# Optimization experiments

Hardware: AMD Instinct MI355X
Metric: run time of the kernel (lower is better)

## Reference

```python
import jax, jax.numpy as jnp
import numpy as np

S, N, H = 1024, 64, 1024  # source len, batch, hidden_size
INPUT_SIZE = 1024         # attention projection dim (linear1/linear2 out)


def setup_inputs() -> dict:
    key = jax.random.key(0)
    ks = jax.random.split(key, 8)
    sc_h = 1.0 / np.sqrt(H)
    sc_i = 1.0 / np.sqrt(INPUT_SIZE)
    return {
        "out_e": jax.random.normal(ks[0], (S, N, H), dtype=jnp.float32),
        "hidden_d": jax.random.normal(ks[1], (1, N, H), dtype=jnp.float32),
        # torch Linear weights are [out_features, in_features]
        "W1": jax.random.uniform(ks[2], (INPUT_SIZE, H), jnp.float32, -sc_h, sc_h),
        "b1": jax.random.uniform(ks[3], (INPUT_SIZE,), jnp.float32, -sc_h, sc_h),
        "W2": jax.random.uniform(ks[4], (INPUT_SIZE, H), jnp.float32, -sc_h, sc_h),
        "b2": jax.random.uniform(ks[5], (INPUT_SIZE,), jnp.float32, -sc_h, sc_h),
        "W3": jax.random.uniform(ks[6], (1, INPUT_SIZE), jnp.float32, -sc_i, sc_i),
        "b3": jax.random.uniform(ks[7], (1,), jnp.float32, -sc_i, sc_i),
    }


def reference(out_e, hidden_d, W1, b1, W2, b2, W3, b3):
    # hidden_d [1,N,H] broadcast to [S,N,H] (torch .repeat)
    s = out_e.shape[0]
    hd = jnp.broadcast_to(hidden_d, (s,) + hidden_d.shape[1:])
    # a: [S,N,1] = linear3(tanh(linear1(hd) + linear2(out_e)))
    e = jnp.tanh(hd @ W1.T + b1 + out_e @ W2.T + b2)
    a = e @ W3.T + b3
    # softmax over the source dim (dim=0 in torch)
    alpha = jax.nn.softmax(a, axis=0)          # [S,N,1]
    c = jnp.einsum('sne,snh->enh', alpha, out_e)  # [1,N,H]
    return (c, alpha)
```

## Files before the change

kernel.cpp:

```cpp
#include <hip/hip_runtime.h>
#include <hip/hip_fp16.h>

#define S_LEN 1024
#define N_B   64
#define H_DIM 1024
#define I_DIM 1024

typedef __attribute__((ext_vector_type(8))) _Float16 half8;
typedef __attribute__((ext_vector_type(4))) _Float16 half4;
typedef __attribute__((ext_vector_type(4))) float    f32x4;

__device__ __forceinline__ void gload16(const void* g, void* l) {
  __builtin_amdgcn_global_load_lds(
      (const __attribute__((address_space(1))) unsigned int*)g,
      (__attribute__((address_space(3))) unsigned int*)l, 16, 0, 0);
}

__global__ void cvt_f32_f16(const float* __restrict__ src,
                            _Float16* __restrict__ dst, int n8) {
  int idx = blockIdx.x * blockDim.x + threadIdx.x;
  int stride = gridDim.x * blockDim.x;
  const float4* s4 = (const float4*)src;
  half8* d8 = (half8*)dst;
  for (int i = idx; i < n8; i += stride) {
    float4 a = s4[2 * i], b = s4[2 * i + 1];
    half8 h;
    h[0] = (_Float16)a.x; h[1] = (_Float16)a.y;
    h[2] = (_Float16)a.z; h[3] = (_Float16)a.w;
    h[4] = (_Float16)b.x; h[5] = (_Float16)b.y;
    h[6] = (_Float16)b.z; h[7] = (_Float16)b.w;
    d8[i] = h;
  }
}

__global__ void u1_kernel(const float* __restrict__ hd,
                          const float* __restrict__ W1,
                          const float* __restrict__ b1,
                          const float* __restrict__ b2,
                          float* __restrict__ u1,
                          float* __restrict__ a_ws) {
  __shared__ float hs[4 * 1024];
  int nb = blockIdx.x & 15;
  int ib = blockIdx.x >> 4;
  int t = threadIdx.x;
  int n0 = nb * 4;

  a_ws[blockIdx.x * 256 + t] = 0.f;

  const float4* g4 = (const float4*)(hd + (size_t)n0 * 1024);
  float4* h4 = (float4*)hs;
#pragma unroll
  for (int r = 0; r < 4; ++r) h4[r * 256 + t] = g4[r * 256 + t];
  __syncthreads();

  int il = t >> 2, q = t & 3;
  int i = ib * 64 + il;
  const float4* w4 = (const float4*)(W1 + (size_t)i * 1024 + q * 256);
  float s0 = 0.f, s1 = 0.f, s2 = 0.f, s3 = 0.f;
  for (int hh = 0; hh < 64; ++hh) {
    float4 wv = w4[hh];
    int hb = q * 256 + hh * 4;
    float4 v0 = *(const float4*)&hs[0 * 1024 + hb];
    float4 v1 = *(const float4*)&hs[1 * 1024 + hb];
    float4 v2 = *(const float4*)&hs[2 * 1024 + hb];
    float4 v3 = *(const float4*)&hs[3 * 1024 + hb];
    s0 += wv.x * v0.x + wv.y * v0.y + wv.z * v0.z + wv.w * v0.w;
    s1 += wv.x * v1.x + wv.y * v1.y + wv.z * v1.z + wv.w * v1.w;
    s2 += wv.x * v2.x + wv.y * v2.y + wv.z * v2.z + wv.w * v2.w;
    s3 += wv.x * v3.x + wv.y * v3.y + wv.z * v3.z + wv.w * v3.w;
  }
  s0 += __shfl_xor(s0, 1); s0 += __shfl_xor(s0, 2);
  s1 += __shfl_xor(s1, 1); s1 += __shfl_xor(s1, 2);
  s2 += __shfl_xor(s2, 1); s2 += __shfl_xor(s2, 2);
  s3 += __shfl_xor(s3, 1); s3 += __shfl_xor(s3, 2);
  if (q == 0) {
    float bb = b1[i] + b2[i];
    u1[(size_t)(n0 + 0) * 1024 + i] = s0 + bb;
    u1[(size_t)(n0 + 1) * 1024 + i] = s1 + bb;
    u1[(size_t)(n0 + 2) * 1024 + i] = s2 + bb;
    u1[(size_t)(n0 + 3) * 1024 + i] = s3 + bb;
  }
}

__global__ __launch_bounds__(256) void fused_gemm_tanh(
    const _Float16* __restrict__ A,
    const _Float16* __restrict__ B,
    const float* __restrict__ u1,
    const float* __restrict__ W3,
    float* __restrict__ a_ws)
{
  __shared__ __align__(16) _Float16 As[2][128 * 32];
  __shared__ __align__(16) _Float16 Bs[2][128 * 32];

  const int t = threadIdx.x;
  const int lane = t & 63;
  const int w = t >> 6;
  const int wr = w >> 1, wc = w & 1;
  const int bx = blockIdx.x;
  const int xcd = bx & 7;
  const int j = bx >> 3;
  const int rb = xcd + ((j >> 3) << 3);
  const int cb = j & 7;
  const int m0 = rb * 128, i0 = cb * 128;

  const int strow = t >> 2;
  const int stcol = ((t & 3) ^ ((t >> 2) & 3)) * 8;
  const _Float16* gA = A + (size_t)(m0 + strow) * 1024 + stcol;
  const _Float16* gB = B + (size_t)(i0 + strow) * 1024 + stcol;
  const int ldsoff = strow * 32 + (t & 3) * 8;

  f32x4 acc[4][4] = {};

  gload16(gA,             &As[0][ldsoff]);
  gload16(gA + 64 * 1024, &As[0][ldsoff + 64 * 32]);
  gload16(gB,             &Bs[0][ldsoff]);
  gload16(gB + 64 * 1024, &Bs[0][ldsoff + 64 * 32]);
  __syncthreads();

  const int fr = lane & 15;
  const int kg = lane >> 4;
  const int un = (kg ^ (fr & 3)) * 8;
  const int aoff = (wr * 64 + fr) * 32 + un;
  const int boff = (wc * 64 + fr) * 32 + un;

  for (int kt = 0; kt < 32; ++kt) {
    const int buf = kt & 1;
    if (kt < 31) {
      const _Float16* gA2 = gA + (kt + 1) * 32;
      const _Float16* gB2 = gB + (kt + 1) * 32;
      gload16(gA2,             &As[buf ^ 1][ldsoff]);
      gload16(gA2 + 64 * 1024, &As[buf ^ 1][ldsoff + 64 * 32]);
      gload16(gB2,             &Bs[buf ^ 1][ldsoff]);
      gload16(gB2 + 64 * 1024, &Bs[buf ^ 1][ldsoff + 64 * 32]);
    }
    half8 af[4], bf[4];
#pragma unroll
    for (int mi = 0; mi < 4; ++mi)
      af[mi] = *(const half8*)&As[buf][aoff + mi * 16 * 32];
#pragma unroll
    for (int ni = 0; ni < 4; ++ni)
      bf[ni] = *(const half8*)&Bs[buf][boff + ni * 16 * 32];
#pragma unroll
    for (int mi = 0; mi < 4; ++mi)
#pragma unroll
      for (int ni = 0; ni < 4; ++ni)
        acc[mi][ni] = __builtin_amdgcn_mfma_f32_16x16x32_f16(
            af[mi], bf[ni], acc[mi][ni], 0, 0, 0);
    __syncthreads();
  }

  float w3v[4];
#pragma unroll
  for (int ni = 0; ni < 4; ++ni)
    w3v[ni] = W3[i0 + wc * 64 + ni * 16 + fr];

#pragma unroll
  for (int mi = 0; mi < 4; ++mi) {
#pragma unroll
    for (int jj = 0; jj < 4; ++jj) {
      int m = m0 + wr * 64 + mi * 16 + kg * 4 + jj;
      int n = m & 63;
      const float* u1row = u1 + (size_t)n * 1024 + i0 + wc * 64;
      float s = 0.f;
#pragma unroll
      for (int ni = 0; ni < 4; ++ni) {
        float e = acc[mi][ni][jj] + u1row[ni * 16 + fr];
        float th = 1.f - 2.f / (__expf(2.f * e) + 1.f);
        s += th * w3v[ni];
      }
      s += __shfl_xor(s, 1);
      s += __shfl_xor(s, 2);
      s += __shfl_xor(s, 4);
      s += __shfl_xor(s, 8);
      if (fr == 0) atomicAdd(&a_ws[m], s);
    }
  }
}

__global__ void softmax_col(const float* __restrict__ a_ws,
                            float* __restrict__ alpha,
                            float* __restrict__ c_out) {
  int n = blockIdx.x;
  int t = threadIdx.x;
  __shared__ float red[256];
#pragma unroll
  for (int q = 0; q < 4; ++q) c_out[(size_t)n * 1024 + q * 256 + t] = 0.f;
  float v[4];
  float mx = -1e30f;
#pragma unroll
  for (int q = 0; q < 4; ++q) {
    v[q] = a_ws[(size_t)(t + q * 256) * 64 + n];
    mx = fmaxf(mx, v[q]);
  }
  red[t] = mx; __syncthreads();
  for (int off = 128; off > 0; off >>= 1) {
    if (t < off) red[t] = fmaxf(red[t], red[t + off]);
    __syncthreads();
  }
  mx = red[0];
  __syncthreads();
  float sum = 0.f;
#pragma unroll
  for (int q = 0; q < 4; ++q) { v[q] = __expf(v[q] - mx); sum += v[q]; }
  red[t] = sum; __syncthreads();
  for (int off = 128; off > 0; off >>= 1) {
    if (t < off) red[t] += red[t + off];
    __syncthreads();
  }
  float inv = 1.f / red[0];
#pragma unroll
  for (int q = 0; q < 4; ++q)
    alpha[(size_t)(t + q * 256) * 64 + n] = v[q] * inv;
}

__global__ void weighted_sum(const _Float16* __restrict__ oe,
                             const float* __restrict__ alpha,
                             float* __restrict__ cout) {
  int n = blockIdx.x & 63;
  int sc = blockIdx.x >> 6;
  int t = threadIdx.x;
  __shared__ float al[64];
  if (t < 64) al[t] = alpha[(size_t)(sc * 64 + t) * 64 + n];
  __syncthreads();
  float a0 = 0.f, a1 = 0.f, a2 = 0.f, a3 = 0.f;
#pragma unroll 4
  for (int sl = 0; sl < 64; ++sl) {
    float a = al[sl];
    int s = sc * 64 + sl;
    half4 x = *(const half4*)(oe + (size_t)(s * 64 + n) * 1024 + t * 4);
    a0 += a * (float)x[0]; a1 += a * (float)x[1];
    a2 += a * (float)x[2]; a3 += a * (float)x[3];
  }
  float* c = cout + (size_t)n * 1024 + t * 4;
  atomicAdd(c + 0, a0);
  atomicAdd(c + 1, a1);
  atomicAdd(c + 2, a2);
  atomicAdd(c + 3, a3);
}

extern "C" void kernel_launch(void* const* d_in, const int* in_sizes, int n_in,
                              void* d_out, int out_size, void* d_ws,
                              size_t ws_size, hipStream_t stream) {
  const float* out_e    = (const float*)d_in[0];
  const float* hidden_d = (const float*)d_in[1];
  const float* W1       = (const float*)d_in[2];
  const float* b1       = (const float*)d_in[3];
  const float* W2       = (const float*)d_in[4];
  const float* b2       = (const float*)d_in[5];
  const float* W3       = (const float*)d_in[6];

  char* ws = (char*)d_ws;
  _Float16* oe16 = (_Float16*)ws;
  _Float16* w216 = (_Float16*)(ws + 134217728);
  float* u1   = (float*)(ws + 134217728 + 2097152);
  float* a_ws = (float*)(ws + 134217728 + 2097152 + 262144);

  float* c_out = (float*)d_out;
  float* alpha = (float*)d_out + 65536;

  hipLaunchKernelGGL(cvt_f32_f16, dim3(4096), dim3(256), 0, stream,
                     out_e, oe16, 67108864 / 8);
  hipLaunchKernelGGL(cvt_f32_f16, dim3(512), dim3(256), 0, stream,
                     W2, w216, 1048576 / 8);
  hipLaunchKernelGGL(u1_kernel, dim3(256), dim3(256), 0, stream,
                     hidden_d, W1, b1, b2, u1, a_ws);
  hipLaunchKernelGGL(fused_gemm_tanh, dim3(4096), dim3(256), 0, stream,
                     oe16, w216, u1, W3, a_ws);
  hipLaunchKernelGGL(softmax_col, dim3(64), dim3(256), 0, stream,
                     a_ws, alpha, c_out);
  hipLaunchKernelGGL(weighted_sum, dim3(1024), dim3(256), 0, stream,
                     oe16, alpha, c_out);
}
```

Before: 666.4 us.

## Merge setup kernels, fuse softmax into weighted sum, drop LDS swizzle

Folds the two f32-to-f16 conversions and the u1 projection into one setup launch, which also zeroes c_out. Softmax is now fused into the weighted-sum kernel: each of the 1024 blocks recomputes the column max and sum redundantly and writes its own 64-entry alpha slice. The XOR swizzle on the GEMM's LDS staging and fragment reads is removed. This cuts the launch count from six to three, but risks LDS bank conflicts in the GEMM and adds redundant softmax reductions.

```diff
diff --git a/kernel.cpp b/kernel.cpp
--- a/kernel.cpp
+++ b/kernel.cpp
@@ -16,36 +16,56 @@
       (__attribute__((address_space(3))) unsigned int*)l, 16, 0, 0);
 }
 
-__global__ void cvt_f32_f16(const float* __restrict__ src,
-                            _Float16* __restrict__ dst, int n8) {
-  int idx = blockIdx.x * blockDim.x + threadIdx.x;
-  int stride = gridDim.x * blockDim.x;
-  const float4* s4 = (const float4*)src;
-  half8* d8 = (half8*)dst;
-  for (int i = idx; i < n8; i += stride) {
-    float4 a = s4[2 * i], b = s4[2 * i + 1];
-    half8 h;
-    h[0] = (_Float16)a.x; h[1] = (_Float16)a.y;
-    h[2] = (_Float16)a.z; h[3] = (_Float16)a.w;
-    h[4] = (_Float16)b.x; h[5] = (_Float16)b.y;
-    h[6] = (_Float16)b.z; h[7] = (_Float16)b.w;
-    d8[i] = h;
-  }
-}
-
-__global__ void u1_kernel(const float* __restrict__ hd,
-                          const float* __restrict__ W1,
-                          const float* __restrict__ b1,
-                          const float* __restrict__ b2,
-                          float* __restrict__ u1,
-                          float* __restrict__ a_ws) {
+__global__ __launch_bounds__(256) void setup_kernel(
+    const float* __restrict__ out_e, const float* __restrict__ hd,
+    const float* __restrict__ W1, const float* __restrict__ b1,
+    const float* __restrict__ b2, const float* __restrict__ W2,
+    _Float16* __restrict__ oe16, _Float16* __restrict__ w216,
+    float* __restrict__ u1, float* __restrict__ a_ws,
+    float* __restrict__ c_out) {
   __shared__ float hs[4 * 1024];
-  int nb = blockIdx.x & 15;
-  int ib = blockIdx.x >> 4;
-  int t = threadIdx.x;
-  int n0 = nb * 4;
-
-  a_ws[blockIdx.x * 256 + t] = 0.f;
+  const int bx = blockIdx.x;
+  const int t = threadIdx.x;
+
+  if (bx < 4096) {
+    const float4* s4 = (const float4*)out_e;
+    half8* d8 = (half8*)oe16;
+    int i = bx * 256 + t;
+#pragma unroll
+    for (int r = 0; r < 8; ++r, i += 1048576) {
+      float4 a = s4[2 * i], b = s4[2 * i + 1];
+      half8 h;
+      h[0] = (_Float16)a.x; h[1] = (_Float16)a.y;
+      h[2] = (_Float16)a.z; h[3] = (_Float16)a.w;
+      h[4] = (_Float16)b.x; h[5] = (_Float16)b.y;
+      h[6] = (_Float16)b.z; h[7] = (_Float16)b.w;
+      d8[i] = h;
+    }
+    return;
+  }
+  if (bx < 4160) {
+    const float4* s4 = (const float4*)W2;
+    half8* d8 = (half8*)w216;
+    int i = (bx - 4096) * 256 + t;
+#pragma unroll
+    for (int r = 0; r < 8; ++r, i += 16384) {
+      float4 a = s4[2 * i], b = s4[2 * i + 1];
+      half8 h;
+      h[0] = (_Float16)a.x; h[1] = (_Float16)a.y;
+      h[2] = (_Float16)a.z; h[3] = (_Float16)a.w;
+      h[4] = (_Float16)b.x; h[5] = (_Float16)b.y;
+      h[6] = (_Float16)b.z; h[7] = (_Float16)b.w;
+      d8[i] = h;
+    }
+    return;
+  }
+  const int local = bx - 4160;
+  a_ws[local * 256 + t] = 0.f;
+  c_out[local * 256 + t] = 0.f;
+
+  const int nb = local & 15;
+  const int ib = local >> 4;
+  const int n0 = nb * 4;
 
   const float4* g4 = (const float4*)(hd + (size_t)n0 * 1024);
   float4* h4 = (float4*)hs;
@@ -104,10 +124,10 @@
   const int m0 = rb * 128, i0 = cb * 128;
 
   const int strow = t >> 2;
-  const int stcol = ((t & 3) ^ ((t >> 2) & 3)) * 8;
+  const int stcol = (t & 3) * 8;
   const _Float16* gA = A + (size_t)(m0 + strow) * 1024 + stcol;
   const _Float16* gB = B + (size_t)(i0 + strow) * 1024 + stcol;
-  const int ldsoff = strow * 32 + (t & 3) * 8;
+  const int ldsoff = strow * 32 + stcol;
 
   f32x4 acc[4][4] = {};
 
@@ -119,9 +139,8 @@
 
   const int fr = lane & 15;
   const int kg = lane >> 4;
-  const int un = (kg ^ (fr & 3)) * 8;
-  const int aoff = (wr * 64 + fr) * 32 + un;
-  const int boff = (wc * 64 + fr) * 32 + un;
+  const int aoff = (wr * 64 + fr) * 32 + kg * 8;
+  const int boff = (wc * 64 + fr) * 32 + kg * 8;
 
   for (int kt = 0; kt < 32; ++kt) {
     const int buf = kt & 1;
@@ -177,14 +196,15 @@
   }
 }
 
-__global__ void softmax_col(const float* __restrict__ a_ws,
-                            float* __restrict__ alpha,
-                            float* __restrict__ c_out) {
-  int n = blockIdx.x;
-  int t = threadIdx.x;
+__global__ __launch_bounds__(256) void softmax_wsum(
+    const float* __restrict__ a_ws, const _Float16* __restrict__ oe,
+    float* __restrict__ alpha, float* __restrict__ cout) {
+  const int n = blockIdx.x & 63;
+  const int sc = blockIdx.x >> 6;
+  const int t = threadIdx.x;
   __shared__ float red[256];
-#pragma unroll
-  for (int q = 0; q < 4; ++q) c_out[(size_t)n * 1024 + q * 256 + t] = 0.f;
+  __shared__ float al[64];
+
   float v[4];
   float mx = -1e30f;
 #pragma unroll
@@ -207,21 +227,17 @@
     if (t < off) red[t] += red[t + off];
     __syncthreads();
   }
-  float inv = 1.f / red[0];
-#pragma unroll
-  for (int q = 0; q < 4; ++q)
-    alpha[(size_t)(t + q * 256) * 64 + n] = v[q] * inv;
-}
-
-__global__ void weighted_sum(const _Float16* __restrict__ oe,
-                             const float* __restrict__ alpha,
-                             float* __restrict__ cout) {
-  int n = blockIdx.x & 63;
-  int sc = blockIdx.x >> 6;
-  int t = threadIdx.x;
-  __shared__ float al[64];
-  if (t < 64) al[t] = alpha[(size_t)(sc * 64 + t) * 64 + n];
-  __syncthreads();
+  const float inv = 1.f / red[0];
+
+  const int q0 = sc >> 2;
+  const int tlo = (sc & 3) * 64;
+  if (t >= tlo && t < tlo + 64) {
+    float a = v[q0] * inv;
+    al[t - tlo] = a;
+    alpha[(size_t)(sc * 64 + (t - tlo)) * 64 + n] = a;
+  }
+  __syncthreads();
+
   float a0 = 0.f, a1 = 0.f, a2 = 0.f, a3 = 0.f;
 #pragma unroll 4
   for (int sl = 0; sl < 64; ++sl) {
@@ -258,16 +274,11 @@
   float* c_out = (float*)d_out;
   float* alpha = (float*)d_out + 65536;
 
-  hipLaunchKernelGGL(cvt_f32_f16, dim3(4096), dim3(256), 0, stream,
-                     out_e, oe16, 67108864 / 8);
-  hipLaunchKernelGGL(cvt_f32_f16, dim3(512), dim3(256), 0, stream,
-                     W2, w216, 1048576 / 8);
-  hipLaunchKernelGGL(u1_kernel, dim3(256), dim3(256), 0, stream,
-                     hidden_d, W1, b1, b2, u1, a_ws);
+  hipLaunchKernelGGL(setup_kernel, dim3(4416), dim3(256), 0, stream,
+                     out_e, hidden_d, W1, b1, b2, W2,
+                     oe16, w216, u1, a_ws, c_out);
   hipLaunchKernelGGL(fused_gemm_tanh, dim3(4096), dim3(256), 0, stream,
                      oe16, w216, u1, W3, a_ws);
-  hipLaunchKernelGGL(softmax_col, dim3(64), dim3(256), 0, stream,
-                     a_ws, alpha, c_out);
-  hipLaunchKernelGGL(weighted_sum, dim3(1024), dim3(256), 0, stream,
-                     oe16, alpha, c_out);
-}
+  hipLaunchKernelGGL(softmax_wsum, dim3(1024), dim3(256), 0, stream,
+                     a_ws, oe16, alpha, c_out);
+}
```

Result: faster. 648.4 us (-2.7%).
